# Kernel optimization log

Measured on AMD Instinct MI355X. Metric: run time of the kernel, lower is better.

The kernel has to match this reference:

```python
import jax, jax.numpy as jnp
import numpy as np

L, D, H, F = 6, 1024, 8, 2048
B, S, IN = 4, 2048, 128
DK = D // H
EPS = 1e-6


def layer_norm(x, s, b):
    mu = jnp.mean(x, -1, keepdims=True)
    var = jnp.mean((x - mu) ** 2, -1, keepdims=True)
    return (x - mu) * jax.lax.rsqrt(var + EPS) * s + b


def rotate_every_two(x):
    x1 = x[..., ::2]
    x2 = x[..., 1::2]
    return jnp.stack([-x2, x1], axis=-1).reshape(x.shape)


def rotary_tables():
    # torchscale RetNet xpos-style angles: each freq repeated twice (interleaved)
    angle = 1.0 / (10000.0 ** jnp.linspace(0.0, 1.0, DK // 2))
    angle = jnp.repeat(angle, 2)                      # [DK]
    idx = jnp.arange(S, dtype=jnp.float32)[:, None]   # [S,1]
    return jnp.sin(idx * angle), jnp.cos(idx * angle)  # [S,DK] each


def decay_mask():
    # gamma_h = 1 - 2^(-5-h); D[h,n,m] = gamma_h^(n-m) for n>=m else 0,
    # row-normalized by sqrt(row sum) as in torchscale.
    gamma = 1.0 - 2.0 ** (-5.0 - jnp.arange(H, dtype=jnp.float32))  # [H]
    n = jnp.arange(S)
    diff = jnp.clip(n[:, None] - n[None, :], 0)                      # [S,S]
    tril = n[:, None] >= n[None, :]
    m = jnp.where(tril[None], gamma[:, None, None] ** diff[None].astype(jnp.float32), 0.0)
    return m / jnp.sqrt(jnp.sum(m, -1, keepdims=True))               # [H,S,S]


def setup_inputs() -> dict:
    key = jax.random.key(0)
    ks = iter(jax.random.split(key, 24))
    p = lambda shape: jax.random.normal(next(ks), shape, jnp.float32) * 0.02
    return {
        "x": jax.random.normal(next(ks), (B, S, IN), jnp.float32),
        "W_in": p((IN, D)), "b_in": jnp.zeros((D,), jnp.float32),
        "Wq": p((L, D, D)), "Wk": p((L, D, D)), "Wv": p((L, D, D)),
        "Wg": p((L, D, D)), "Wo": p((L, D, D)),
        "gn_g": jnp.ones((L, D), jnp.float32),
        "ln1_s": jnp.ones((L, D), jnp.float32), "ln1_b": jnp.zeros((L, D), jnp.float32),
        "ffn_W1": p((L, D, F)), "ffn_b1": jnp.zeros((L, F), jnp.float32),
        "ffn_W2": p((L, F, D)), "ffn_b2": jnp.zeros((L, D), jnp.float32),
        "ln2_s": jnp.ones((L, D), jnp.float32), "ln2_b": jnp.zeros((L, D), jnp.float32),
        "lnf_s": jnp.ones((D,), jnp.float32), "lnf_b": jnp.zeros((D,), jnp.float32),
        "W_reg": p((D, 1)), "b_reg": jnp.zeros((1,), jnp.float32),
    }


def reference(x, W_in, b_in, Wq, Wk, Wv, Wg, Wo, gn_g, ln1_s, ln1_b,
              ffn_W1, ffn_b1, ffn_W2, ffn_b2, ln2_s, ln2_b, lnf_s, lnf_b,
              W_reg, b_reg):
    sin, cos = rotary_tables()
    dmask = decay_mask()  # [H,S,S]
    h = x @ W_in + b_in   # input_embed
    for l in range(L):
        # --- multi-scale retention (pre-norm) ---
        y = layer_norm(h, ln1_s[l], ln1_b[l])
        q = (y @ Wq[l]).reshape(B, S, H, DK).transpose(0, 2, 1, 3)
        k = (y @ Wk[l]).reshape(B, S, H, DK).transpose(0, 2, 1, 3) * (DK ** -0.5)
        v = (y @ Wv[l]).reshape(B, S, H, DK).transpose(0, 2, 1, 3)
        q = q * cos + rotate_every_two(q) * sin
        k = k * cos + rotate_every_two(k) * sin
        scores = jnp.einsum('bhnd,bhmd->bhnm', q, k)
        ret = scores * dmask[None]
        ret = ret / jnp.clip(jnp.abs(ret).sum(-1, keepdims=True), 1.0, None)
        o = jnp.einsum('bhnm,bhmd->bhnd', ret, v)
        # per-head group (RMS) norm
        o = o * jax.lax.rsqrt(jnp.mean(o * o, -1, keepdims=True) + EPS)
        o = o.transpose(0, 2, 1, 3).reshape(B, S, D) * gn_g[l]
        g = y @ Wg[l]
        h = h + (jax.nn.silu(g) * o) @ Wo[l]
        # --- FFN (pre-norm) ---
        y = layer_norm(h, ln2_s[l], ln2_b[l])
        h = h + jax.nn.gelu(y @ ffn_W1[l] + ffn_b1[l]) @ ffn_W2[l] + ffn_b2[l]
    h = layer_norm(h, lnf_s, lnf_b)
    out = 1.1 * jax.nn.sigmoid(h @ W_reg + b_reg) - 0.05
    return out.squeeze(-1)  # [B,S]
```

## Files before the change

kernel.cpp:

```cpp
#include <hip/hip_runtime.h>

#define L_ 6
#define D_ 1024
#define H_ 8
#define F_ 2048
#define B_ 4
#define S_ 2048
#define IN_ 128
#define DK_ 128
#define BS_ (B_*S_)
#define D2_ 4096

typedef short bf16x8 __attribute__((ext_vector_type(8)));
typedef float f32x4 __attribute__((ext_vector_type(4)));

__device__ inline float b2f(unsigned short u){ union{unsigned int i; float f;} v; v.i = ((unsigned int)u)<<16; return v.f; }
__device__ inline unsigned short f2b(float f){ union{unsigned int i; float f;} v; v.f = f; unsigned int r = v.i + 0x7FFFu + ((v.i>>16)&1u); return (unsigned short)(r>>16); }
__device__ inline unsigned int cvtpk(float lo, float hi){
    unsigned int r; asm("v_cvt_pk_bf16_f32 %0, %1, %2" : "=v"(r) : "v"(lo), "v"(hi)); return r;
}

__device__ inline void gld16(const void* g, void* l) {
    __builtin_amdgcn_global_load_lds((const __attribute__((address_space(1))) unsigned int*)g,
                                     (__attribute__((address_space(3))) unsigned int*)l, 16, 0, 0);
}

#define GBAR() do{ asm volatile("" ::: "memory"); __builtin_amdgcn_s_barrier(); asm volatile("" ::: "memory"); }while(0)

__global__ void f32_to_bf16_k(const float* __restrict__ in, unsigned short* __restrict__ out, int n)
{
    int i = blockIdx.x*256 + threadIdx.x;
    if (i < n) out[i] = f2b(in[i]);
}

__global__ void transpose_w_k(const float* __restrict__ in, unsigned short* __restrict__ out, int R, int C, size_t ostride)
{
    __shared__ float tile[32][33];
    int z = blockIdx.z;
    const float* pi = in + (size_t)z*R*C;
    unsigned short* po = out + (size_t)z*ostride;
    int c0 = blockIdx.x*32, r0 = blockIdx.y*32;
    int tx = threadIdx.x, ty = threadIdx.y;
    #pragma unroll
    for (int i=0;i<4;i++) tile[ty+i*8][tx] = pi[(size_t)(r0+ty+i*8)*C + c0+tx];
    __syncthreads();
    #pragma unroll
    for (int i=0;i<4;i++) po[(size_t)(c0+ty+i*8)*R + r0+tx] = f2b(tile[tx][ty+i*8]);
}

__global__ void transpose_v_k(const unsigned short* __restrict__ vb, unsigned short* __restrict__ vT)
{
    __shared__ unsigned short tile[32][33];
    int z = blockIdx.z;
    int b = z >> 3, hh = z & 7;
    int s0 = blockIdx.x*32, d0 = blockIdx.y*32;
    int tx = threadIdx.x, ty = threadIdx.y;
    #pragma unroll
    for (int i=0;i<4;i++) tile[ty+i*8][tx] = vb[(size_t)(b*S_ + s0+ty+i*8)*D2_ + hh*DK_ + d0+tx];
    __syncthreads();
    #pragma unroll
    for (int i=0;i<4;i++) vT[((size_t)z*DK_ + d0+ty+i*8)*S_ + s0+tx] = tile[tx][ty+i*8];
}

__global__ void build_sincos_k(float* __restrict__ cost, float* __restrict__ sint)
{
    int id = blockIdx.x*256 + threadIdx.x;
    int s = id >> 6, i = id & 63;
    float ang = powf(10000.f, -(float)i/63.f);
    float a = (float)s * ang;
    float sv = sinf(a), cv = cosf(a);
    sint[s*DK_ + 2*i] = sv; sint[s*DK_ + 2*i+1] = sv;
    cost[s*DK_ + 2*i] = cv; cost[s*DK_ + 2*i+1] = cv;
}

__global__ void build_dnorm_k(float* __restrict__ dnorm)
{
    int id = blockIdx.x*256 + threadIdx.x;
    int h = id >> 11, n = id & (S_-1);
    double g = 1.0 - exp2((double)(-5 - h));
    double sum = (1.0 - exp(((double)(n+1))*log(g))) / (1.0 - g);
    dnorm[id] = (float)(1.0/sqrt(sum));
}

__device__ inline float bsum(float v, float* red, int t)
{
    #pragma unroll
    for (int m=32; m; m>>=1) v += __shfl_xor(v, m);
    __syncthreads();
    if ((t & 63) == 0) red[t>>6] = v;
    __syncthreads();
    return red[0]+red[1]+red[2]+red[3];
}

__global__ __launch_bounds__(256) void ln_to_bf16_k(const float* __restrict__ x, const float* __restrict__ s,
                                                    const float* __restrict__ b, unsigned short* __restrict__ y)
{
    __shared__ float red[4];
    int row = blockIdx.x, t = threadIdx.x;
    const float* xr = x + (size_t)row * D_;
    float4 v = ((const float4*)xr)[t];
    float mu = bsum(v.x+v.y+v.z+v.w, red, t) * (1.f/D_);
    float d0=v.x-mu, d1=v.y-mu, d2=v.z-mu, d3=v.w-mu;
    float var = bsum(d0*d0+d1*d1+d2*d2+d3*d3, red, t) * (1.f/D_);
    float inv = rsqrtf(var + 1e-6f);
    int c = t*4;
    float o0 = d0*inv*s[c+0] + b[c+0];
    float o1 = d1*inv*s[c+1] + b[c+1];
    float o2 = d2*inv*s[c+2] + b[c+2];
    float o3 = d3*inv*s[c+3] + b[c+3];
    unsigned long long pk = (unsigned long long)f2b(o0) | ((unsigned long long)f2b(o1)<<16)
                          | ((unsigned long long)f2b(o2)<<32) | ((unsigned long long)f2b(o3)<<48);
    *(unsigned long long*)(y + (size_t)row*D_ + c) = pk;
}

template<int MODE, int BN>
__global__ __launch_bounds__(512, 2) void gemm3(const unsigned short* __restrict__ A,
                                                const unsigned short* __restrict__ Bt,
                                                const float* __restrict__ bias,
                                                void* __restrict__ Cv,
                                                int M, int N, int K)
{
    constexpr int NR  = BN/64;
    constexpr int ASZ = 256*64;
    constexpr int BSZ = BN*64;
    __shared__ unsigned char lds[4*ASZ + 4*BSZ];

    const int tid = threadIdx.x, lane = tid & 63, w = tid >> 6;
    const int r16 = lane & 15, quad = (lane >> 4) & 3;
    const int wm = w >> 2, wn = w & 3;
    const int m0 = blockIdx.y * 256, n0 = blockIdx.x * BN;

    const int srow = tid >> 2;
    const int schk = (tid & 3) ^ ((tid >> 3) & 3);
    const unsigned short* gA = A  + (size_t)(m0 + srow) * K + schk*8;
    const unsigned short* gB = Bt + (size_t)(n0 + srow) * K + schk*8;

    const int rchk = (quad ^ ((r16 >> 1) & 3)) * 16;
    const int aoff = (wm*128 + r16)*64 + rchk;
    const int boff = (wn*(BN/4) + r16)*64 + rchk;

    f32x4 acc[8][NR];
    #pragma unroll
    for (int i=0;i<8;i++)
      #pragma unroll
      for (int j=0;j<NR;j++) acc[i][j] = (f32x4){0.f,0.f,0.f,0.f};

    const int NT = K >> 5;

    auto stage = [&](int t){
        const int bf = t & 3;
        const size_t ko = (size_t)t * 32;
        gld16(gA + ko,                 lds + bf*ASZ + w*1024);
        gld16(gA + ko + (size_t)128*K, lds + bf*ASZ + 8192 + w*1024);
        gld16(gB + ko,                 lds + 4*ASZ + bf*BSZ + w*1024);
        if constexpr (BN == 256)
            gld16(gB + ko + (size_t)128*K, lds + 4*ASZ + bf*BSZ + 8192 + w*1024);
    };

    auto compute = [&](int t){
        const unsigned char* ab = lds + (t&3)*ASZ;
        const unsigned char* bb = lds + 4*ASZ + (t&3)*BSZ;
        bf16x8 af[8], bg[NR];
        #pragma unroll
        for (int i=0;i<8;i++) af[i] = *(const bf16x8*)(ab + aoff + i*1024);
        #pragma unroll
        for (int j=0;j<NR;j++) bg[j] = *(const bf16x8*)(bb + boff + j*1024);
        __builtin_amdgcn_s_setprio(1);
        #pragma unroll
        for (int i=0;i<8;i++)
          #pragma unroll
          for (int j=0;j<NR;j++)
            acc[i][j] = __builtin_amdgcn_mfma_f32_16x16x32_bf16(af[i], bg[j], acc[i][j], 0,0,0);
        __builtin_amdgcn_s_setprio(0);
    };

    stage(0); stage(1); stage(2);

    for (int t = 0; t + 3 < NT; ++t) {
        stage(t + 3);
        if constexpr (BN == 256) asm volatile("s_waitcnt vmcnt(12)" ::: "memory");
        else                     asm volatile("s_waitcnt vmcnt(9)"  ::: "memory");
        GBAR();
        compute(t);
        GBAR();
    }
    if constexpr (BN == 256) asm volatile("s_waitcnt vmcnt(8)" ::: "memory");
    else                     asm volatile("s_waitcnt vmcnt(6)" ::: "memory");
    GBAR(); compute(NT-3); GBAR();
    if constexpr (BN == 256) asm volatile("s_waitcnt vmcnt(4)" ::: "memory");
    else                     asm volatile("s_waitcnt vmcnt(3)" ::: "memory");
    GBAR(); compute(NT-2); GBAR();
    asm volatile("s_waitcnt vmcnt(0)" ::: "memory");
    GBAR(); compute(NT-1);

    float* Cf = (float*)Cv;
    unsigned short* Cb = (unsigned short*)Cv;
    #pragma unroll
    for (int j=0;j<NR;j++) {
      const int ccol = n0 + wn*(BN/4) + j*16 + r16;
      const float bv = bias ? bias[ccol] : 0.f;
      #pragma unroll
      for (int i=0;i<8;i++) {
        #pragma unroll
        for (int r=0;r<4;r++) {
          const int crow = m0 + wm*128 + i*16 + quad*4 + r;
          float v = acc[i][j][r];
          if (MODE == 0) { Cf[(size_t)crow*N + ccol] = v + bv; }
          else if (MODE == 1) { Cf[(size_t)crow*N + ccol] += v + bv; }
          else if (MODE == 2) { Cb[(size_t)crow*N + ccol] = f2b(v); }
          else {
            v += bv;
            float t3 = tanhf(0.7978845608028654f*(v + 0.044715f*v*v*v));
            Cb[(size_t)crow*N + ccol] = f2b(0.5f*v*(1.f + t3));
          }
        }
      }
    }
}

__global__ __launch_bounds__(256) void rope_qk_k(unsigned short* __restrict__ qkvg,
                                                 const float* __restrict__ cost, const float* __restrict__ sint)
{
    int id = blockIdx.x*256 + threadIdx.x;
    int row = id >> 9;
    int d = (id & 511) * 2;
    int s = row & (S_-1);
    int dk = d & (DK_-1);
    float c0 = cost[s*DK_ + dk],   s0 = sint[s*DK_ + dk];
    float c1 = cost[s*DK_ + dk+1], s1 = sint[s*DK_ + dk+1];
    size_t off = (size_t)row*D2_ + d;
    unsigned int qu = *(unsigned int*)(qkvg + off);
    float q0 = b2f((unsigned short)(qu & 0xffffu)), q1 = b2f((unsigned short)(qu >> 16));
    float r0 = q0*c0 - q1*s0;
    float r1 = q1*c1 + q0*s1;
    *(unsigned int*)(qkvg + off) = (unsigned int)f2b(r0) | ((unsigned int)f2b(r1) << 16);
    const float sc = 0.08838834764831845f;
    unsigned int ku = *(unsigned int*)(qkvg + off + 1024);
    float k0 = b2f((unsigned short)(ku & 0xffffu))*sc, k1 = b2f((unsigned short)(ku >> 16))*sc;
    float t0 = k0*c0 - k1*s0;
    float t1 = k1*c1 + k0*s1;
    *(unsigned int*)(qkvg + off + 1024) = (unsigned int)f2b(t0) | ((unsigned int)f2b(t1) << 16);
}

__global__ __launch_bounds__(256, 2) void retention_k(const unsigned short* __restrict__ qk_base,
    const unsigned short* __restrict__ vT, const float* __restrict__ dnorm,
    const float* __restrict__ gng, unsigned short* __restrict__ attnin)
{
    __shared__ __align__(16) unsigned char lds[75776];
    const int pr = blockIdx.x;
    const int bh = blockIdx.y;
    const int b = bh >> 3, hh = bh & 7;
    const int tid = threadIdx.x, lane = tid & 63, w = tid >> 6;
    const int r16 = lane & 15, quad = lane >> 4;

    const float l2g = log2f(1.f - exp2f(-5.f - (float)hh));
    const int ithr = (int)(45.f / (-l2g));
    const unsigned int mkr = (r16 & 7) << 4;

    const int mk2  = ((tid >> 4) & 7) << 4;
    const int mkv2 = ((tid >> 3) & 7) << 4;
    const unsigned short* ksrc = qk_base + 1024 + ((size_t)(b*S_) + (tid>>4))*D2_ + hh*DK_
                                + ((((tid&15)*16) ^ mk2) >> 1);
    const unsigned short* vsrc = vT + ((size_t)bh*DK_ + (tid>>3))*S_ + ((((tid&7)*16) ^ mkv2) >> 1);

    float Aarr[4];
    #pragma unroll
    for (int r=0;r<4;r++) Aarr[r] = exp2f(l2g * (float)(63 - (w*16 + quad*4 + r)));

    float* dsums = (float*)(lds + 73728);
    float* ssums = (float*)(lds + 74752);

    auto stage = [&](int c2, int kt2){
        const unsigned short* s0 = ksrc + (size_t)kt2*64*D2_;
        #pragma unroll
        for (int i=0;i<4;i++)
            gld16(s0 + (size_t)i*16*D2_, lds + c2*16384 + i*4096 + w*1024);
        const unsigned short* s1 = vsrc + kt2*64;
        #pragma unroll
        for (int j=0;j<4;j++)
            gld16(s1 + (size_t)j*32*S_, lds + 32768 + c2*16384 + j*4096 + w*1024);
    };

    int cur = 0;

    #pragma unroll 1
    for (int seg = 0; seg < 2; ++seg) {
        const int qt = seg ? pr : (31 - pr);
        const int n0 = qt * 64;
        const int kt_start = max(0, (n0 - ithr) >> 6);

        bf16x8 qf[4][4];
        const unsigned short* qptr = qk_base + ((size_t)(b*S_ + n0 + r16))*D2_ + hh*DK_;
        #pragma unroll
        for (int qtl=0;qtl<4;qtl++)
          #pragma unroll
          for (int c=0;c<4;c++) qf[qtl][c] = *(const bf16x8*)(qptr + qtl*16*D2_ + c*32 + quad*8);

        f32x4 oacc[4][2];
        #pragma unroll
        for (int qtl=0;qtl<4;qtl++)
          #pragma unroll
          for (int dt=0;dt<2;dt++) oacc[qtl][dt] = (f32x4){0.f,0.f,0.f,0.f};
        float dsum[4] = {0.f,0.f,0.f,0.f};

        stage(cur, kt_start);

        #pragma unroll 1
        for (int kt = kt_start; kt <= qt; ++kt) {
            if (kt < qt) { stage(cur^1, kt+1); asm volatile("s_waitcnt vmcnt(8)" ::: "memory"); }
            else         { asm volatile("s_waitcnt vmcnt(0)" ::: "memory"); }
            GBAR();

            const unsigned char* kb = lds + cur*16384;
            bf16x8 kf[4];
            #pragma unroll
            for (int c=0;c<4;c++)
                kf[c] = *(const bf16x8*)(kb + (w*16 + r16)*256 + ((c*64 + quad*16) ^ mkr));
            f32x4 sf[4];
            #pragma unroll
            for (int qtl=0;qtl<4;qtl++) sf[qtl] = (f32x4){0.f,0.f,0.f,0.f};
            __builtin_amdgcn_s_setprio(1);
            #pragma unroll
            for (int c=0;c<4;c++)
              #pragma unroll
              for (int qtl=0;qtl<4;qtl++)
                sf[qtl] = __builtin_amdgcn_mfma_f32_16x16x32_bf16(kf[c], qf[qtl][c], sf[qtl], 0,0,0);
            __builtin_amdgcn_s_setprio(0);

            const bool diag = (kt == qt);
            #pragma unroll
            for (int qtl=0;qtl<4;qtl++) {
                float Bq = exp2f(l2g * (float)(n0 + qtl*16 + r16 - kt*64 - 63));
                float pv[4];
                #pragma unroll
                for (int r=0;r<4;r++) {
                    float p = sf[qtl][r] * Aarr[r] * Bq;
                    if (diag && (w*16 + quad*4 + r > qtl*16 + r16)) p = 0.f;
                    dsum[qtl] += fabsf(p);
                    pv[r] = p;
                }
                unsigned long long pk = (unsigned long long)cvtpk(pv[0], pv[1])
                                      | ((unsigned long long)cvtpk(pv[2], pv[3]) << 32);
                *(unsigned long long*)(lds + 65536 + (qtl*16 + r16)*128 + ((w*32 + quad*8) ^ mkr)) = pk;
            }
            asm volatile("s_waitcnt lgkmcnt(0)" ::: "memory");
            GBAR();

            const unsigned char* vb = lds + 32768 + cur*16384;
            bf16x8 pa[4][2], vf[2][2];
            #pragma unroll
            for (int qtl=0;qtl<4;qtl++)
              #pragma unroll
              for (int ks=0;ks<2;ks++)
                pa[qtl][ks] = *(const bf16x8*)(lds + 65536 + (qtl*16 + r16)*128 + ((ks*64 + quad*16) ^ mkr));
            #pragma unroll
            for (int dt=0;dt<2;dt++)
              #pragma unroll
              for (int ks=0;ks<2;ks++)
                vf[dt][ks] = *(const bf16x8*)(vb + (w*32 + dt*16 + r16)*128 + ((ks*64 + quad*16) ^ mkr));
            __builtin_amdgcn_s_setprio(1);
            #pragma unroll
            for (int qtl=0;qtl<4;qtl++)
              #pragma unroll
              for (int dt=0;dt<2;dt++)
                #pragma unroll
                for (int ks=0;ks<2;ks++)
                  oacc[qtl][dt] = __builtin_amdgcn_mfma_f32_16x16x32_bf16(pa[qtl][ks], vf[dt][ks], oacc[qtl][dt], 0,0,0);
            __builtin_amdgcn_s_setprio(0);
            GBAR();
            cur ^= 1;
        }

        #pragma unroll
        for (int qtl=0;qtl<4;qtl++) {
            float dv = dsum[qtl];
            dv += __shfl_xor(dv, 16); dv += __shfl_xor(dv, 32);
            if (lane < 16) dsums[w*64 + qtl*16 + r16] = dv;
        }
        __syncthreads();
        float scl[4][4], pss[4][4];
        #pragma unroll
        for (int qtl=0;qtl<4;qtl++) {
            #pragma unroll
            for (int r=0;r<4;r++) {
                int nl = qtl*16 + quad*4 + r;
                float dv = dsums[nl] + dsums[64+nl] + dsums[128+nl] + dsums[192+nl];
                float nr = dnorm[hh*S_ + n0 + nl];
                float sc = nr / fmaxf(1.f, dv * nr);
                scl[qtl][r] = sc;
                float s2 = 0.f;
                #pragma unroll
                for (int dt=0;dt<2;dt++) { float t = oacc[qtl][dt][r]*sc; s2 += t*t; }
                s2 += __shfl_xor(s2,1); s2 += __shfl_xor(s2,2);
                s2 += __shfl_xor(s2,4); s2 += __shfl_xor(s2,8);
                pss[qtl][r] = s2;
            }
        }
        if (r16 == 0) {
            #pragma unroll
            for (int qtl=0;qtl<4;qtl++)
              #pragma unroll
              for (int r=0;r<4;r++)
                ssums[w*64 + qtl*16 + quad*4 + r] = pss[qtl][r];
        }
        __syncthreads();
        #pragma unroll
        for (int qtl=0;qtl<4;qtl++) {
            float rms[4];
            #pragma unroll
            for (int r=0;r<4;r++) {
                int nl = qtl*16 + quad*4 + r;
                float s2 = ssums[nl] + ssums[64+nl] + ssums[128+nl] + ssums[192+nl];
                rms[r] = rsqrtf(s2*(1.f/DK_) + 1e-6f);
            }
            #pragma unroll
            for (int dt=0;dt<2;dt++) {
                int d = w*32 + dt*16 + r16;
                float gg = gng[hh*DK_ + d];
                #pragma unroll
                for (int r=0;r<4;r++) {
                    int n = n0 + qtl*16 + quad*4 + r;
                    float gv = b2f(qk_base[(size_t)(b*S_ + n)*D2_ + 3072 + hh*DK_ + d]);
                    float sg = gv / (1.f + expf(-gv));
                    float ov = oacc[qtl][dt][r]*scl[qtl][r]*rms[r]*gg;
                    attnin[(size_t)(b*S_ + n)*D_ + hh*DK_ + d] = f2b(ov*sg);
                }
            }
        }
        __syncthreads();
    }
}

__global__ __launch_bounds__(256) void head_out_k(const float* __restrict__ h, const float* __restrict__ s,
    const float* __restrict__ b, const float* __restrict__ wreg, const float* __restrict__ breg,
    float* __restrict__ out)
{
    __shared__ float red[4];
    int row = blockIdx.x, t = threadIdx.x;
    const float* xr = h + (size_t)row*D_;
    float4 v = ((const float4*)xr)[t];
    float mu = bsum(v.x+v.y+v.z+v.w, red, t) * (1.f/D_);
    float d0=v.x-mu, d1=v.y-mu, d2=v.z-mu, d3=v.w-mu;
    float var = bsum(d0*d0+d1*d1+d2*d2+d3*d3, red, t) * (1.f/D_);
    float inv = rsqrtf(var + 1e-6f);
    int c = t*4;
    float dot = (d0*inv*s[c+0]+b[c+0])*wreg[c+0] + (d1*inv*s[c+1]+b[c+1])*wreg[c+1]
              + (d2*inv*s[c+2]+b[c+2])*wreg[c+2] + (d3*inv*s[c+3]+b[c+3])*wreg[c+3];
    dot = bsum(dot, red, t);
    if (t == 0) out[row] = 1.1f / (1.f + expf(-(dot + breg[0]))) - 0.05f;
}

extern "C" void kernel_launch(void* const* d_in, const int* in_sizes, int n_in,
                              void* d_out, int out_size, void* d_ws, size_t ws_size,
                              hipStream_t stream)
{
    (void)in_sizes; (void)n_in; (void)out_size; (void)ws_size;
    const float* x    = (const float*)d_in[0];
    const float* W_in = (const float*)d_in[1];
    const float* b_in = (const float*)d_in[2];
    const float* Wq   = (const float*)d_in[3];
    const float* Wk   = (const float*)d_in[4];
    const float* Wv   = (const float*)d_in[5];
    const float* Wg   = (const float*)d_in[6];
    const float* Wo   = (const float*)d_in[7];
    const float* gn_g = (const float*)d_in[8];
    const float* ln1s = (const float*)d_in[9];
    const float* ln1b = (const float*)d_in[10];
    const float* W1   = (const float*)d_in[11];
    const float* b1   = (const float*)d_in[12];
    const float* W2   = (const float*)d_in[13];
    const float* b2   = (const float*)d_in[14];
    const float* ln2s = (const float*)d_in[15];
    const float* ln2b = (const float*)d_in[16];
    const float* lnfs = (const float*)d_in[17];
    const float* lnfb = (const float*)d_in[18];
    const float* Wreg = (const float*)d_in[19];
    const float* breg = (const float*)d_in[20];

    char* ws = (char*)d_ws;
    size_t off = 0;
    auto alloc = [&](size_t bytes) { char* p = ws + off; off += (bytes + 255) & ~(size_t)255; return p; };

    const size_t DD = (size_t)D_*D_;
    unsigned short* wqkvgT = (unsigned short*)alloc((size_t)L_*4*DD*2);
    unsigned short* woT  = (unsigned short*)alloc((size_t)L_*DD*2);
    unsigned short* w1T  = (unsigned short*)alloc((size_t)L_*D_*F_*2);
    unsigned short* w2T  = (unsigned short*)alloc((size_t)L_*D_*F_*2);
    unsigned short* winT = (unsigned short*)alloc((size_t)D_*IN_*2);
    unsigned short* x_bf = (unsigned short*)alloc((size_t)BS_*IN_*2);
    float*          hbuf = (float*)alloc((size_t)BS_*D_*4);
    unsigned short* y_bf = (unsigned short*)alloc((size_t)BS_*D_*2);
    unsigned short* qkvg = (unsigned short*)alloc((size_t)BS_*D2_*2);
    unsigned short* vTb  = (unsigned short*)alloc((size_t)BS_*D_*2);
    float*          cost = (float*)alloc((size_t)S_*DK_*4);
    float*          sint = (float*)alloc((size_t)S_*DK_*4);
    float*          dnrm = (float*)alloc((size_t)H_*S_*4);
    unsigned short* attn = y_bf;
    unsigned short* midb = qkvg;

    dim3 tb(32, 8);

    f32_to_bf16_k<<<(BS_*IN_)/256, 256, 0, stream>>>(x, x_bf, BS_*IN_);
    transpose_w_k<<<dim3(32,32,L_), tb, 0, stream>>>(Wq, wqkvgT + 0*DD, D_, D_, 4*DD);
    transpose_w_k<<<dim3(32,32,L_), tb, 0, stream>>>(Wk, wqkvgT + 1*DD, D_, D_, 4*DD);
    transpose_w_k<<<dim3(32,32,L_), tb, 0, stream>>>(Wv, wqkvgT + 2*DD, D_, D_, 4*DD);
    transpose_w_k<<<dim3(32,32,L_), tb, 0, stream>>>(Wg, wqkvgT + 3*DD, D_, D_, 4*DD);
    transpose_w_k<<<dim3(32,32,L_), tb, 0, stream>>>(Wo, woT, D_, D_, DD);
    transpose_w_k<<<dim3(64,32,L_), tb, 0, stream>>>(W1, w1T, D_, F_, (size_t)D_*F_);
    transpose_w_k<<<dim3(32,64,L_), tb, 0, stream>>>(W2, w2T, F_, D_, (size_t)D_*F_);
    transpose_w_k<<<dim3(32, 4, 1), tb, 0, stream>>>(W_in, winT, IN_, D_, (size_t)D_*IN_);
    build_sincos_k<<<(S_*64)/256, 256, 0, stream>>>(cost, sint);
    build_dnorm_k<<<(H_*S_)/256, 256, 0, stream>>>(dnrm);

    gemm3<0,128><<<dim3(D_/128, BS_/256), 512, 0, stream>>>(x_bf, winT, b_in, hbuf, BS_, D_, IN_);

    for (int l = 0; l < L_; ++l) {
        ln_to_bf16_k<<<BS_, 256, 0, stream>>>(hbuf, ln1s + l*D_, ln1b + l*D_, y_bf);
        gemm3<2,256><<<dim3(D2_/256, BS_/256), 512, 0, stream>>>(y_bf, wqkvgT + (size_t)l*4*DD, nullptr, qkvg, BS_, D2_, D_);
        rope_qk_k<<<(BS_*D_/2)/256, 256, 0, stream>>>(qkvg, cost, sint);
        transpose_v_k<<<dim3(S_/32, DK_/32, B_*H_), tb, 0, stream>>>(qkvg + 2048, vTb);
        retention_k<<<dim3(16, B_*H_), 256, 0, stream>>>(qkvg, vTb, dnrm, gn_g + l*D_, attn);
        gemm3<1,128><<<dim3(D_/128, BS_/256), 512, 0, stream>>>(attn, woT + (size_t)l*DD, nullptr, hbuf, BS_, D_, D_);
        ln_to_bf16_k<<<BS_, 256, 0, stream>>>(hbuf, ln2s + l*D_, ln2b + l*D_, y_bf);
        gemm3<3,256><<<dim3(F_/256, BS_/256), 512, 0, stream>>>(y_bf, w1T + (size_t)l*D_*F_, b1 + l*F_, midb, BS_, F_, D_);
        gemm3<1,128><<<dim3(D_/128, BS_/256), 512, 0, stream>>>(midb, w2T + (size_t)l*D_*F_, b2 + l*D_, hbuf, BS_, D_, F_);
    }

    head_out_k<<<BS_, 256, 0, stream>>>(hbuf, lnfs, lnfb, Wreg, breg, (float*)d_out);
}
```

Measured before the change: 2.246 ms.

## Generalize GEMM tiling, use double-buffered LDS, and add XCD-aware block remapping

Replaces the fixed 256-row, 4-stage GEMM with a template over block tile and warp layout. It uses a 2-stage LDS double buffer and remaps block IDs so consecutive blocks spread across the 8 XCDs. Smaller N=1024 and FFN1 GEMMs now launch 128x128 or 256x128 tiles with 256 threads, giving more blocks and higher occupancy. The cost is less prefetch depth and possibly lower per-block reuse.

```diff
diff --git a/kernel.cpp b/kernel.cpp
--- a/kernel.cpp
+++ b/kernel.cpp
@@ -113,22 +113,34 @@
     *(unsigned long long*)(y + (size_t)row*D_ + c) = pk;
 }
 
-template<int MODE, int BN>
-__global__ __launch_bounds__(512, 2) void gemm3(const unsigned short* __restrict__ A,
-                                                const unsigned short* __restrict__ Bt,
-                                                const float* __restrict__ bias,
-                                                void* __restrict__ Cv,
-                                                int M, int N, int K)
-{
-    constexpr int NR  = BN/64;
-    constexpr int ASZ = 256*64;
+template<int MODE, int BM, int BN, int WMC, int WNC>
+__global__ __launch_bounds__(WMC*WNC*64, ((BM/WMC)*(BN/WNC) >= 128*64) ? 2 : 3)
+void gemm4(const unsigned short* __restrict__ A,
+           const unsigned short* __restrict__ Bt,
+           const float* __restrict__ bias,
+           void* __restrict__ Cv,
+           int M, int N, int K)
+{
+    constexpr int THR = WMC*WNC*64;
+    constexpr int IR  = BM/WMC/16;
+    constexpr int JR  = BN/WNC/16;
+    constexpr int ASZ = BM*64;
     constexpr int BSZ = BN*64;
-    __shared__ unsigned char lds[4*ASZ + 4*BSZ];
+    constexpr int RP  = THR/4;
+    constexpr int AP  = BM/RP;
+    constexpr int BP  = BN/RP;
+    constexpr int Sa  = AP + BP;
+    __shared__ unsigned char lds[2*(ASZ+BSZ)];
 
     const int tid = threadIdx.x, lane = tid & 63, w = tid >> 6;
     const int r16 = lane & 15, quad = (lane >> 4) & 3;
-    const int wm = w >> 2, wn = w & 3;
-    const int m0 = blockIdx.y * 256, n0 = blockIdx.x * BN;
+    const int wm = w / WNC, wn = w % WNC;
+
+    const int nwg = (int)(gridDim.x * gridDim.y);
+    int bid = (int)(blockIdx.y * gridDim.x + blockIdx.x);
+    if ((nwg & 7) == 0) bid = (bid & 7) * (nwg >> 3) + (bid >> 3);
+    const int m0 = (bid / (int)gridDim.x) * BM;
+    const int n0 = (bid % (int)gridDim.x) * BN;
 
     const int srow = tid >> 2;
     const int schk = (tid & 3) ^ ((tid >> 3) & 3);
@@ -136,74 +148,71 @@
     const unsigned short* gB = Bt + (size_t)(n0 + srow) * K + schk*8;
 
     const int rchk = (quad ^ ((r16 >> 1) & 3)) * 16;
-    const int aoff = (wm*128 + r16)*64 + rchk;
-    const int boff = (wn*(BN/4) + r16)*64 + rchk;
-
-    f32x4 acc[8][NR];
-    #pragma unroll
-    for (int i=0;i<8;i++)
+    const int aoff = (wm*(BM/WMC) + r16)*64 + rchk;
+    const int boff = (wn*(BN/WNC) + r16)*64 + rchk;
+
+    f32x4 acc[IR][JR];
+    #pragma unroll
+    for (int i=0;i<IR;i++)
       #pragma unroll
-      for (int j=0;j<NR;j++) acc[i][j] = (f32x4){0.f,0.f,0.f,0.f};
+      for (int j=0;j<JR;j++) acc[i][j] = (f32x4){0.f,0.f,0.f,0.f};
 
     const int NT = K >> 5;
 
     auto stage = [&](int t){
-        const int bf = t & 3;
+        unsigned char* la = lds + (t&1)*(ASZ+BSZ);
+        unsigned char* lb = la + ASZ;
         const size_t ko = (size_t)t * 32;
-        gld16(gA + ko,                 lds + bf*ASZ + w*1024);
-        gld16(gA + ko + (size_t)128*K, lds + bf*ASZ + 8192 + w*1024);
-        gld16(gB + ko,                 lds + 4*ASZ + bf*BSZ + w*1024);
-        if constexpr (BN == 256)
-            gld16(gB + ko + (size_t)128*K, lds + 4*ASZ + bf*BSZ + 8192 + w*1024);
+        #pragma unroll
+        for (int p=0;p<AP;p++)
+            gld16(gA + ko + (size_t)(p*RP)*K, la + p*RP*64 + tid*16);
+        #pragma unroll
+        for (int p=0;p<BP;p++)
+            gld16(gB + ko + (size_t)(p*RP)*K, lb + p*RP*64 + tid*16);
     };
 
     auto compute = [&](int t){
-        const unsigned char* ab = lds + (t&3)*ASZ;
-        const unsigned char* bb = lds + 4*ASZ + (t&3)*BSZ;
-        bf16x8 af[8], bg[NR];
-        #pragma unroll
-        for (int i=0;i<8;i++) af[i] = *(const bf16x8*)(ab + aoff + i*1024);
-        #pragma unroll
-        for (int j=0;j<NR;j++) bg[j] = *(const bf16x8*)(bb + boff + j*1024);
+        const unsigned char* ab = lds + (t&1)*(ASZ+BSZ);
+        const unsigned char* bb = ab + ASZ;
+        bf16x8 af[IR], bg[JR];
+        #pragma unroll
+        for (int i=0;i<IR;i++) af[i] = *(const bf16x8*)(ab + aoff + i*1024);
+        #pragma unroll
+        for (int j=0;j<JR;j++) bg[j] = *(const bf16x8*)(bb + boff + j*1024);
         __builtin_amdgcn_s_setprio(1);
         #pragma unroll
-        for (int i=0;i<8;i++)
+        for (int i=0;i<IR;i++)
           #pragma unroll
-          for (int j=0;j<NR;j++)
+          for (int j=0;j<JR;j++)
             acc[i][j] = __builtin_amdgcn_mfma_f32_16x16x32_bf16(af[i], bg[j], acc[i][j], 0,0,0);
         __builtin_amdgcn_s_setprio(0);
     };
 
-    stage(0); stage(1); stage(2);
-
-    for (int t = 0; t + 3 < NT; ++t) {
-        stage(t + 3);
-        if constexpr (BN == 256) asm volatile("s_waitcnt vmcnt(12)" ::: "memory");
-        else                     asm volatile("s_waitcnt vmcnt(9)"  ::: "memory");
+    stage(0);
+    for (int t = 0; t < NT; ++t) {
+        if (t + 1 < NT) {
+            stage(t + 1);
+            if constexpr (Sa == 4) asm volatile("s_waitcnt vmcnt(4)" ::: "memory");
+            else                   asm volatile("s_waitcnt vmcnt(6)" ::: "memory");
+        } else {
+            asm volatile("s_waitcnt vmcnt(0)" ::: "memory");
+        }
         GBAR();
         compute(t);
         GBAR();
     }
-    if constexpr (BN == 256) asm volatile("s_waitcnt vmcnt(8)" ::: "memory");
-    else                     asm volatile("s_waitcnt vmcnt(6)" ::: "memory");
-    GBAR(); compute(NT-3); GBAR();
-    if constexpr (BN == 256) asm volatile("s_waitcnt vmcnt(4)" ::: "memory");
-    else                     asm volatile("s_waitcnt vmcnt(3)" ::: "memory");
-    GBAR(); compute(NT-2); GBAR();
-    asm volatile("s_waitcnt vmcnt(0)" ::: "memory");
-    GBAR(); compute(NT-1);
 
     float* Cf = (float*)Cv;
     unsigned short* Cb = (unsigned short*)Cv;
     #pragma unroll
-    for (int j=0;j<NR;j++) {
-      const int ccol = n0 + wn*(BN/4) + j*16 + r16;
+    for (int j=0;j<JR;j++) {
+      const int ccol = n0 + wn*(BN/WNC) + j*16 + r16;
       const float bv = bias ? bias[ccol] : 0.f;
       #pragma unroll
-      for (int i=0;i<8;i++) {
+      for (int i=0;i<IR;i++) {
         #pragma unroll
         for (int r=0;r<4;r++) {
-          const int crow = m0 + wm*128 + i*16 + quad*4 + r;
+          const int crow = m0 + wm*(BM/WMC) + i*16 + quad*4 + r;
           float v = acc[i][j][r];
           if (MODE == 0) { Cf[(size_t)crow*N + ccol] = v + bv; }
           else if (MODE == 1) { Cf[(size_t)crow*N + ccol] += v + bv; }
@@ -512,18 +521,18 @@
     build_sincos_k<<<(S_*64)/256, 256, 0, stream>>>(cost, sint);
     build_dnorm_k<<<(H_*S_)/256, 256, 0, stream>>>(dnrm);
 
-    gemm3<0,128><<<dim3(D_/128, BS_/256), 512, 0, stream>>>(x_bf, winT, b_in, hbuf, BS_, D_, IN_);
+    gemm4<0,128,128,2,2><<<dim3(D_/128, BS_/128), 256, 0, stream>>>(x_bf, winT, b_in, hbuf, BS_, D_, IN_);
 
     for (int l = 0; l < L_; ++l) {
         ln_to_bf16_k<<<BS_, 256, 0, stream>>>(hbuf, ln1s + l*D_, ln1b + l*D_, y_bf);
-        gemm3<2,256><<<dim3(D2_/256, BS_/256), 512, 0, stream>>>(y_bf, wqkvgT + (size_t)l*4*DD, nullptr, qkvg, BS_, D2_, D_);
+        gemm4<2,256,256,2,4><<<dim3(D2_/256, BS_/256), 512, 0, stream>>>(y_bf, wqkvgT + (size_t)l*4*DD, nullptr, qkvg, BS_, D2_, D_);
         rope_qk_k<<<(BS_*D_/2)/256, 256, 0, stream>>>(qkvg, cost, sint);
         transpose_v_k<<<dim3(S_/32, DK_/32, B_*H_), tb, 0, stream>>>(qkvg + 2048, vTb);
         retention_k<<<dim3(16, B_*H_), 256, 0, stream>>>(qkvg, vTb, dnrm, gn_g + l*D_, attn);
-        gemm3<1,128><<<dim3(D_/128, BS_/256), 512, 0, stream>>>(attn, woT + (size_t)l*DD, nullptr, hbuf, BS_, D_, D_);
+        gemm4<1,128,128,2,2><<<dim3(D_/128, BS_/128), 256, 0, stream>>>(attn, woT + (size_t)l*DD, nullptr, hbuf, BS_, D_, D_);
         ln_to_bf16_k<<<BS_, 256, 0, stream>>>(hbuf, ln2s + l*D_, ln2b + l*D_, y_bf);
-        gemm3<3,256><<<dim3(F_/256, BS_/256), 512, 0, stream>>>(y_bf, w1T + (size_t)l*D_*F_, b1 + l*F_, midb, BS_, F_, D_);
-        gemm3<1,128><<<dim3(D_/128, BS_/256), 512, 0, stream>>>(midb, w2T + (size_t)l*D_*F_, b2 + l*D_, hbuf, BS_, D_, F_);
+        gemm4<3,256,128,2,2><<<dim3(F_/128, BS_/256), 256, 0, stream>>>(y_bf, w1T + (size_t)l*D_*F_, b1 + l*F_, midb, BS_, F_, D_);
+        gemm4<1,128,128,2,2><<<dim3(D_/128, BS_/128), 256, 0, stream>>>(midb, w2T + (size_t)l*D_*F_, b2 + l*D_, hbuf, BS_, D_, F_);
     }
 
     head_out_k<<<BS_, 256, 0, stream>>>(hbuf, lnfs, lnfb, Wreg, breg, (float*)d_out);
```

Result: faster. 2.144 ms (-4.6%).
